# Optimization experiments

Measured on AMD Instinct MI355X. Metric: run time of the kernel, lower is better.

Reference implementation:

```python
import jax, jax.numpy as jnp
import numpy as np

B, P, K = 128, 1024, 4  # 128 clouds of 1024 points, kNN k=4 (includes self, as PyG knn does)


def _edge_mlp(e, W1, b1, W2, b2):
    # PyG MLP([2d, c, c]) with plain_last=True: ReLU after first linear only;
    # batch-norm at init (running_mean=0, var=1) is identity in eval mode.
    h = jax.nn.relu(e @ W1 + b1)
    return h @ W2 + b2


def _dynamic_edge_conv(x, W1, b1, W2, b2):
    # x: [B, P, d]. Recompute kNN graph in feature space per cloud, build edge
    # features [x_i, x_j - x_i], apply MLP, max-aggregate over neighbors.
    sq = jnp.sum(x * x, axis=-1)  # [B,P]
    dist = sq[:, :, None] + sq[:, None, :] - 2.0 * jnp.einsum('bid,bjd->bij', x, x)  # [B,P,P]
    _, idx = jax.lax.top_k(-dist, K)  # [B,P,K] nearest neighbors (self included, dist 0)
    xj = jax.vmap(lambda xc, ic: xc[ic])(x, idx)  # [B,P,K,d]
    xi = jnp.broadcast_to(x[:, :, None, :], xj.shape)
    e = jnp.concatenate([xi, xj - xi], axis=-1)  # [B,P,K,2d]
    h = _edge_mlp(e, W1, b1, W2, b2)  # [B,P,K,c]
    return jnp.max(h, axis=2)  # max aggregation -> [B,P,c]


def setup_inputs() -> dict:
    key = jax.random.key(0)
    ks = jax.random.split(key, 24)
    s = 0.1
    d = {
        'x': jax.random.normal(ks[0], (B * P, 1), dtype=jnp.float32),
        'batch': (jnp.arange(B * P, dtype=jnp.int32) // P),
        # conv1: MLP([2, 32, 32])
        'c1W1': s * jax.random.normal(ks[1], (2, 32)), 'c1b1': jnp.zeros((32,)),
        'c1W2': s * jax.random.normal(ks[2], (32, 32)), 'c1b2': jnp.zeros((32,)),
        # conv2: MLP([64, 32, 32])
        'c2W1': s * jax.random.normal(ks[3], (64, 32)), 'c2b1': jnp.zeros((32,)),
        'c2W2': s * jax.random.normal(ks[4], (32, 32)), 'c2b2': jnp.zeros((32,)),
        # conv3: MLP([64, 64, 64])
        'c3W1': s * jax.random.normal(ks[5], (64, 64)), 'c3b1': jnp.zeros((64,)),
        'c3W2': s * jax.random.normal(ks[6], (64, 64)), 'c3b2': jnp.zeros((64,)),
        # final MLP([128, 264, 264, 264, 2]), norm=None, dropout inactive in eval
        'mW1': s * jax.random.normal(ks[7], (128, 264)), 'mb1': jnp.zeros((264,)),
        'mW2': s * jax.random.normal(ks[8], (264, 264)), 'mb2': jnp.zeros((264,)),
        'mW3': s * jax.random.normal(ks[9], (264, 264)), 'mb3': jnp.zeros((264,)),
        'mW4': s * jax.random.normal(ks[10], (264, 2)), 'mb4': jnp.zeros((2,)),
    }
    return d


def reference(x, batch, c1W1, c1b1, c1W2, c1b2, c2W1, c2b1, c2W2, c2b2,
              c3W1, c3b1, c3W2, c3b2, mW1, mb1, mW2, mb2, mW3, mb3, mW4, mb4):
    # batch ids are contiguous equal-size groups (arange // P); use reshape.
    xb = x.reshape(B, P, -1)
    x1 = _dynamic_edge_conv(xb, c1W1, c1b1, c1W2, c1b2)  # [B,P,32]
    x2 = _dynamic_edge_conv(x1, c2W1, c2b1, c2W2, c2b2)  # [B,P,32]
    x3 = _dynamic_edge_conv(x2, c3W1, c3b1, c3W2, c3b2)  # [B,P,64]
    f = jnp.concatenate([x1, x2, x3], axis=-1).reshape(B * P, -1)  # [N,128]
    h = jax.nn.relu(f @ mW1 + mb1)
    h = jax.nn.relu(h @ mW2 + mb2)
    h = jax.nn.relu(h @ mW3 + mb3)
    out = h @ mW4 + mb4  # [N,2]
    return jax.nn.log_softmax(out, axis=1)
```

## Files before the change

kernel.cpp:

```cpp
#include <hip/hip_runtime.h>
#include <hip/hip_bf16.h>
#include <float.h>
#include <math.h>

#define BB 128
#define PP 1024
#define KNN 4
#define NROWS (BB * PP)

typedef __bf16 v8bf __attribute__((ext_vector_type(8)));
typedef float  v4f  __attribute__((ext_vector_type(4)));

__device__ inline unsigned short f2bs(float f) {
    __hip_bfloat16 h = __float2bfloat16(f);
    return *(unsigned short*)&h;
}
__device__ inline unsigned packbf2(float a, float b) {
    return (unsigned)f2bs(a) | ((unsigned)f2bs(b) << 16);
}
__device__ inline float bflo(unsigned u) { return __builtin_bit_cast(float, u << 16); }
__device__ inline float bfhi(unsigned u) { return __builtin_bit_cast(float, u & 0xFFFF0000u); }

__device__ inline unsigned med3u(unsigned a, unsigned b, unsigned c) {
    unsigned d;
    asm("v_med3_u32 %0, %1, %2, %3" : "=v"(d) : "v"(a), "v"(b), "v"(c));
    return d;
}

__global__ __launch_bounds__(256)
void pack_kernel(const float* __restrict__ src, int D,
                 __hip_bfloat16* __restrict__ xh, __hip_bfloat16* __restrict__ xl,
                 float* __restrict__ sq)
{
    const int t = blockIdx.x * 256 + threadIdx.x;
    const int row = t >> 2, part = t & 3;
    float v[8];
    #pragma unroll
    for (int u = 0; u < 8; u++) {
        int d = part * 8 + u;
        v[u] = (d < D) ? src[(size_t)row * D + d] : 0.f;
    }
    float s = 0.f;
    unsigned int hw[4], lw[4];
    #pragma unroll
    for (int w = 0; w < 4; w++) {
        unsigned short h2[2], l2[2];
        #pragma unroll
        for (int e = 0; e < 2; e++) {
            float x = v[2 * w + e];
            __hip_bfloat16 hb = __float2bfloat16(x);
            float hf = __bfloat162float(hb);
            __hip_bfloat16 lb = __float2bfloat16(x - hf);
            h2[e] = *(unsigned short*)&hb;
            l2[e] = *(unsigned short*)&lb;
            s = fmaf(x, x, s);
        }
        hw[w] = (unsigned int)h2[0] | ((unsigned int)h2[1] << 16);
        lw[w] = (unsigned int)l2[0] | ((unsigned int)l2[1] << 16);
    }
    s += __shfl_xor(s, 1);
    s += __shfl_xor(s, 2);
    uint4 hv; hv.x = hw[0]; hv.y = hw[1]; hv.z = hw[2]; hv.w = hw[3];
    uint4 lv; lv.x = lw[0]; lv.y = lw[1]; lv.z = lw[2]; lv.w = lw[3];
    *(uint4*)&xh[(size_t)row * 32 + part * 8] = hv;
    *(uint4*)&xl[(size_t)row * 32 + part * 8] = lv;
    if (part == 0) sq[row] = s;
}

__global__ __launch_bounds__(256, 4)
void knn_mfma(const __hip_bfloat16* __restrict__ xh, const __hip_bfloat16* __restrict__ xl,
              const float* __restrict__ sq, int* __restrict__ nidx)
{
    __shared__ __align__(16) char scb[64 * 256];
    unsigned* cand = (unsigned*)scb;

    const int tid = threadIdx.x;
    const int wv = tid >> 6, lane = tid & 63;
    const int lr = lane & 15, lq = lane >> 4;
    const int b = blockIdx.y, i0 = blockIdx.x * 64;
    const size_t Rb = (size_t)b * PP;

    v8bf ah[4], al[4];
    #pragma unroll
    for (int it = 0; it < 4; it++) {
        size_t g = Rb + i0 + it * 16 + lr;
        ah[it] = __builtin_bit_cast(v8bf, *(const uint4*)(xh + g * 32 + lq * 8));
        al[it] = __builtin_bit_cast(v8bf, *(const uint4*)(xl + g * 32 + lq * 8));
    }

    float sqq[4][4];
    #pragma unroll
    for (int it = 0; it < 4; it++)
        #pragma unroll
        for (int m = 0; m < 4; m++)
            sqq[it][m] = sq[Rb + i0 + it * 16 + lq * 4 + m];

    const int r = tid & 63, qt = tid >> 6;
    unsigned m0 = ~0u, m1 = ~0u, m2 = ~0u, m3 = ~0u;

    for (int ch = 0; ch < 8; ch++) {
        #pragma unroll
        for (int jt2 = 0; jt2 < 2; jt2++) {
            const int tl = wv * 2 + jt2;
            const size_t gj = Rb + ch * 128 + tl * 16 + lr;
            v8bf bh = __builtin_bit_cast(v8bf, *(const uint4*)(xh + gj * 32 + lq * 8));
            v8bf bl = __builtin_bit_cast(v8bf, *(const uint4*)(xl + gj * 32 + lq * 8));
            const float sqv = sq[gj];
            const unsigned jloc = (unsigned)(ch * 128 + tl * 16 + lr);
            const int cb = wv * 64 + lr * 4;
            #pragma unroll
            for (int it = 0; it < 4; it++) {
                v4f a = (v4f){0.f, 0.f, 0.f, 0.f};
                a = __builtin_amdgcn_mfma_f32_16x16x32_bf16(al[it], bl, a, 0, 0, 0);
                a = __builtin_amdgcn_mfma_f32_16x16x32_bf16(al[it], bh, a, 0, 0, 0);
                a = __builtin_amdgcn_mfma_f32_16x16x32_bf16(ah[it], bl, a, 0, 0, 0);
                a = __builtin_amdgcn_mfma_f32_16x16x32_bf16(ah[it], bh, a, 0, 0, 0);
                #pragma unroll
                for (int m = 0; m < 4; m++) {
                    float s = fmaf(-2.f, a[m], sqv + sqq[it][m]);
                    s = fmaxf(s, 0.f);
                    unsigned key = (__builtin_bit_cast(unsigned, s) & 0xFFFFFC00u) | jloc;
                    const int row = it * 16 + lq * 4 + m;
                    *(unsigned*)(scb + row * 256 + (cb ^ ((row & 7) << 4))) = key;
                }
            }
            __asm__ volatile("" ::: "memory");
            {
                const int rsw = (r & 7) << 4;
                #pragma unroll
                for (int s4 = 0; s4 < 4; s4++) {
                    uint4 kv = *(const uint4*)(scb + r * 256 + ((qt * 64 + s4 * 16) ^ rsw));
                    unsigned kk[4] = {kv.x, kv.y, kv.z, kv.w};
                    #pragma unroll
                    for (int e = 0; e < 4; e++) {
                        unsigned k = kk[e];
                        unsigned n0 = min(m0, k);
                        unsigned n1 = med3u(m0, m1, k);
                        unsigned n2 = med3u(m1, m2, k);
                        unsigned n3 = med3u(m2, m3, k);
                        m0 = n0; m1 = n1; m2 = n2; m3 = n3;
                    }
                }
            }
            __asm__ volatile("" ::: "memory");
        }
    }

    __syncthreads();
    cand[(qt * 4 + 0) * 64 + r] = m0;
    cand[(qt * 4 + 1) * 64 + r] = m1;
    cand[(qt * 4 + 2) * 64 + r] = m2;
    cand[(qt * 4 + 3) * 64 + r] = m3;
    __syncthreads();

    if (tid < 64) {
        unsigned g0 = ~0u, g1 = ~0u, g2 = ~0u, g3 = ~0u;
        #pragma unroll
        for (int s2 = 0; s2 < 16; s2++) {
            unsigned k = cand[s2 * 64 + tid];
            unsigned n0 = min(g0, k);
            unsigned n1 = med3u(g0, g1, k);
            unsigned n2 = med3u(g1, g2, k);
            unsigned n3 = med3u(g2, g3, k);
            g0 = n0; g1 = n1; g2 = n2; g3 = n3;
        }
        const int base = (int)Rb;
        int* op = nidx + (size_t)(Rb + i0 + tid) * KNN;
        op[0] = base + (int)(g0 & 1023u);
        op[1] = base + (int)(g1 & 1023u);
        op[2] = base + (int)(g2 & 1023u);
        op[3] = base + (int)(g3 & 1023u);
    }
}

template<int D, int H, int C, typename OT, bool PACK>
__global__ __launch_bounds__(256, 4)
void edge_mfma(const float* __restrict__ x, const int* __restrict__ nidx,
               const __hip_bfloat16* __restrict__ EW1, const __hip_bfloat16* __restrict__ EW2,
               const float* __restrict__ b1g, const float* __restrict__ b2g,
               OT* __restrict__ out,
               __hip_bfloat16* __restrict__ xhw, __hip_bfloat16* __restrict__ xlw,
               float* __restrict__ sqw)
{
    constexpr int NE = 256;
    constexpr int TDP = (D == 1) ? 32 : 64;
    constexpr int DP  = TDP / 2;
    constexpr int P   = ((TDP > H) ? TDP : H) + 8;
    constexpr int NT1 = H / 16, NT2 = C / 16;
    constexpr int KS1 = TDP / 32, KS2 = H / 32;

    __shared__ __hip_bfloat16 xe[NE * P];

    const int tid = threadIdx.x;
    const int wv = tid >> 6, lane = tid & 63;
    const int lr = lane & 15, q = lane >> 4;
    const int p0 = blockIdx.x * 64;

    {
        const int e = wv * 64 + lane;
        const int j = nidx[(size_t)p0 * KNN + e];
        const int pi = p0 + (e >> 2);
        if constexpr (D == 1) {
            #pragma unroll
            for (int s = 0; s < P / 8; s++) {
                uint4 z; z.x = 0u; z.y = 0u; z.z = 0u; z.w = 0u;
                *(uint4*)&xe[e * P + s * 8] = z;
            }
            xe[e * P + 0]  = __float2bfloat16(x[pi]);
            xe[e * P + DP] = __float2bfloat16(x[j]);
        } else {
            const float* si = x + (size_t)pi * D;
            const float* sj = x + (size_t)j * D;
            #pragma unroll
            for (int s = 0; s < D / 8; s++) {
                float4 f0 = *(const float4*)&si[s * 8];
                float4 f1 = *(const float4*)&si[s * 8 + 4];
                uint4 uv;
                uv.x = packbf2(f0.x, f0.y); uv.y = packbf2(f0.z, f0.w);
                uv.z = packbf2(f1.x, f1.y); uv.w = packbf2(f1.z, f1.w);
                *(uint4*)&xe[e * P + s * 8] = uv;
            }
            #pragma unroll
            for (int s = 0; s < D / 8; s++) {
                float4 f0 = *(const float4*)&sj[s * 8];
                float4 f1 = *(const float4*)&sj[s * 8 + 4];
                uint4 uv;
                uv.x = packbf2(f0.x, f0.y); uv.y = packbf2(f0.z, f0.w);
                uv.z = packbf2(f1.x, f1.y); uv.w = packbf2(f1.z, f1.w);
                *(uint4*)&xe[e * P + DP + s * 8] = uv;
            }
        }
    }

    v4f acc1[4][NT1];
    #pragma unroll
    for (int mi = 0; mi < 4; mi++)
        #pragma unroll
        for (int nt = 0; nt < NT1; nt++) acc1[mi][nt] = (v4f){0.f, 0.f, 0.f, 0.f};

    #pragma unroll
    for (int ks = 0; ks < KS1; ks++) {
        v8bf a[4];
        #pragma unroll
        for (int mi = 0; mi < 4; mi++)
            a[mi] = __builtin_bit_cast(v8bf,
                *(const uint4*)&xe[(wv * 64 + mi * 16 + lr) * P + ks * 32 + q * 8]);
        v8bf b[NT1];
        #pragma unroll
        for (int nt = 0; nt < NT1; nt++)
            b[nt] = __builtin_bit_cast(v8bf,
                *(const uint4*)(EW1 + (size_t)(nt * 16 + lr) * TDP + ks * 32 + q * 8));
        #pragma unroll
        for (int mi = 0; mi < 4; mi++)
            #pragma unroll
            for (int nt = 0; nt < NT1; nt++)
                acc1[mi][nt] = __builtin_amdgcn_mfma_f32_16x16x32_bf16(a[mi], b[nt], acc1[mi][nt], 0, 0, 0);
    }
    #pragma unroll
    for (int nt = 0; nt < NT1; nt++) {
        const float bias = b1g[nt * 16 + lr];
        #pragma unroll
        for (int mi = 0; mi < 4; mi++) {
            #pragma unroll
            for (int m = 0; m < 4; m++) {
                int row = wv * 64 + mi * 16 + q * 4 + m;
                xe[row * P + nt * 16 + lr] =
                    __float2bfloat16(fmaxf(acc1[mi][nt][m] + bias, 0.f));
            }
        }
    }

    v4f acc2[4][NT2];
    #pragma unroll
    for (int mi = 0; mi < 4; mi++)
        #pragma unroll
        for (int nt = 0; nt < NT2; nt++) acc2[mi][nt] = (v4f){0.f, 0.f, 0.f, 0.f};

    #pragma unroll
    for (int ks = 0; ks < KS2; ks++) {
        v8bf a[4];
        #pragma unroll
        for (int mi = 0; mi < 4; mi++)
            a[mi] = __builtin_bit_cast(v8bf,
                *(const uint4*)&xe[(wv * 64 + mi * 16 + lr) * P + ks * 32 + q * 8]);
        v8bf b[NT2];
        #pragma unroll
        for (int nt = 0; nt < NT2; nt++)
            b[nt] = __builtin_bit_cast(v8bf,
                *(const uint4*)(EW2 + (size_t)(nt * 16 + lr) * H + ks * 32 + q * 8));
        #pragma unroll
        for (int mi = 0; mi < 4; mi++)
            #pragma unroll
            for (int nt = 0; nt < NT2; nt++)
                acc2[mi][nt] = __builtin_amdgcn_mfma_f32_16x16x32_bf16(a[mi], b[nt], acc2[mi][nt], 0, 0, 0);
    }
    #pragma unroll
    for (int mi = 0; mi < 4; mi++) {
        const int p = p0 + (wv * 4 + mi) * 4 + q;
        float vs[NT2];
        float ss = 0.f;
        #pragma unroll
        for (int nt = 0; nt < NT2; nt++) {
            const int c = nt * 16 + lr;
            float v = fmaxf(fmaxf(acc2[mi][nt][0], acc2[mi][nt][1]),
                            fmaxf(acc2[mi][nt][2], acc2[mi][nt][3])) + b2g[c];
            vs[nt] = v;
            if constexpr (sizeof(OT) == 4) out[(size_t)p * C + c] = v;
            else                           out[(size_t)p * C + c] = __float2bfloat16(v);
            if constexpr (PACK) ss = fmaf(v, v, ss);
        }
        if constexpr (PACK) {
            ss += __shfl_xor(ss, 1);
            ss += __shfl_xor(ss, 2);
            ss += __shfl_xor(ss, 4);
            ss += __shfl_xor(ss, 8);
            #pragma unroll
            for (int nt = 0; nt < NT2; nt++) {
                float v = vs[nt];
                __hip_bfloat16 hb = __float2bfloat16(v);
                float hf = __bfloat162float(hb);
                __hip_bfloat16 lb = __float2bfloat16(v - hf);
                xhw[(size_t)p * 32 + nt * 16 + lr] = hb;
                xlw[(size_t)p * 32 + nt * 16 + lr] = lb;
            }
            if (lr == 0) sqw[p] = ss;
        }
    }
}

__global__ void prep_kernel(const float* __restrict__ mW1, const float* __restrict__ mW2,
                            const float* __restrict__ mW3,
                            const float* __restrict__ mb1, const float* __restrict__ mb2,
                            const float* __restrict__ mb3,
                            const float* __restrict__ c1W1, const float* __restrict__ c1W2,
                            const float* __restrict__ c2W1, const float* __restrict__ c2W2,
                            const float* __restrict__ c3W1, const float* __restrict__ c3W2,
                            __hip_bfloat16* __restrict__ WT1, __hip_bfloat16* __restrict__ WT2,
                            __hip_bfloat16* __restrict__ WT3, float* __restrict__ bp,
                            __hip_bfloat16* __restrict__ E11, __hip_bfloat16* __restrict__ E12,
                            __hip_bfloat16* __restrict__ E13,
                            __hip_bfloat16* __restrict__ E21, __hip_bfloat16* __restrict__ E22,
                            __hip_bfloat16* __restrict__ E23)
{
    const int t0 = blockIdx.x * blockDim.x + threadIdx.x;
    const int NT = gridDim.x * blockDim.x;
    for (int i = t0; i < 272 * 136; i += NT) {
        int n = i / 136, k = i - n * 136;
        WT1[i] = (n < 264 && k < 128) ? __float2bfloat16(mW1[(size_t)k * 264 + n]) : __float2bfloat16(0.f);
    }
    for (int i = t0; i < 272 * 296; i += NT) {
        int n = i / 296, k = i - n * 296;
        WT2[i] = (n < 264 && k < 264) ? __float2bfloat16(mW2[(size_t)k * 264 + n]) : __float2bfloat16(0.f);
        WT3[i] = (n < 264 && k < 264) ? __float2bfloat16(mW3[(size_t)k * 264 + n]) : __float2bfloat16(0.f);
    }
    for (int i = t0; i < 3 * 272; i += NT) {
        int l = i / 272, n = i - l * 272;
        const float* bsrc = (l == 0) ? mb1 : (l == 1) ? mb2 : mb3;
        bp[i] = (n < 264) ? bsrc[n] : 0.f;
    }
    for (int i = t0; i < 32 * 32; i += NT) {
        int h = i >> 5, k = i & 31;
        float v = (k == 0) ? (c1W1[h] - c1W1[32 + h]) : (k == 16 ? c1W1[32 + h] : 0.f);
        E11[i] = __float2bfloat16(v);
    }
    for (int i = t0; i < 32 * 64; i += NT) {
        int h = i >> 6, k = i & 63;
        float v = (k < 32) ? (c2W1[k * 32 + h] - c2W1[(k + 32) * 32 + h]) : c2W1[k * 32 + h];
        E12[i] = __float2bfloat16(v);
    }
    for (int i = t0; i < 64 * 64; i += NT) {
        int h = i >> 6, k = i & 63;
        float v = (k < 32) ? (c3W1[k * 64 + h] - c3W1[(k + 32) * 64 + h]) : c3W1[k * 64 + h];
        E13[i] = __float2bfloat16(v);
    }
    for (int i = t0; i < 32 * 32; i += NT) {
        int c = i >> 5, h = i & 31;
        E21[i] = __float2bfloat16(c1W2[h * 32 + c]);
        E22[i] = __float2bfloat16(c2W2[h * 32 + c]);
    }
    for (int i = t0; i < 64 * 64; i += NT) {
        int c = i >> 6, h = i & 63;
        E23[i] = __float2bfloat16(c3W2[h * 64 + c]);
    }
}

#define ACT_RB 640

template<int NK>
__device__ __forceinline__ void mlp_layer(
    char* actb, const __hip_bfloat16* __restrict__ WT, const int KP,
    const float* __restrict__ bias, const int wv, const int rlane, const int ph)
{
    v4f acc[2][4], acc16;
    #pragma unroll
    for (int i = 0; i < 2; i++)
        #pragma unroll
        for (int rt = 0; rt < 4; rt++) acc[i][rt] = (v4f){0.f, 0.f, 0.f, 0.f};
    acc16 = (v4f){0.f, 0.f, 0.f, 0.f};

    const int sw = (rlane & 7) << 4;
    const __hip_bfloat16* wbase = WT + (size_t)rlane * KP + ph * 8;
    const bool has16 = (wv >= 4);
    const int r16 = ((wv - 4) & 3) * 16 + rlane;

    v8bf wb[2][2], wb16[2];
    auto loadW = [&](int ks, int buf) {
        wb[buf][0] = __builtin_bit_cast(v8bf,
            *(const uint4*)(wbase + (size_t)wv * 16 * KP + ks * 32));
        wb[buf][1] = __builtin_bit_cast(v8bf,
            *(const uint4*)(wbase + (size_t)(8 + wv) * 16 * KP + ks * 32));
        if (has16)
            wb16[buf] = __builtin_bit_cast(v8bf,
                *(const uint4*)(wbase + (size_t)256 * KP + ks * 32));
    };
    loadW(0, 0);

    #pragma unroll
    for (int ks = 0; ks < NK; ks++) {
        const int cur = ks & 1;
        if (ks + 1 < NK) loadW(ks + 1, cur ^ 1);
        v8bf ab[4], ab16;
        #pragma unroll
        for (int rt = 0; rt < 4; rt++)
            ab[rt] = __builtin_bit_cast(v8bf,
                *(const uint4*)(actb + (rt * 16 + rlane) * ACT_RB + ((ks * 64 + ph * 16) ^ sw)));
        if (has16)
            ab16 = __builtin_bit_cast(v8bf,
                *(const uint4*)(actb + r16 * ACT_RB + ((ks * 64 + ph * 16) ^ sw)));
        #pragma unroll
        for (int i = 0; i < 2; i++)
            #pragma unroll
            for (int rt = 0; rt < 4; rt++)
                acc[i][rt] = __builtin_amdgcn_mfma_f32_16x16x32_bf16(wb[cur][i], ab[rt], acc[i][rt], 0, 0, 0);
        if (has16)
            acc16 = __builtin_amdgcn_mfma_f32_16x16x32_bf16(wb16[cur], ab16, acc16, 0, 0, 0);
    }
    __syncthreads();

    #pragma unroll
    for (int i = 0; i < 2; i++) {
        const int col0 = (wv + 8 * i) * 16 + ph * 4;
        const float4 bv = *(const float4*)&bias[col0];
        #pragma unroll
        for (int rt = 0; rt < 4; rt++) {
            const int row = rt * 16 + rlane;
            ushort4 pk;
            pk.x = f2bs(fmaxf(acc[i][rt][0] + bv.x, 0.f));
            pk.y = f2bs(fmaxf(acc[i][rt][1] + bv.y, 0.f));
            pk.z = f2bs(fmaxf(acc[i][rt][2] + bv.z, 0.f));
            pk.w = f2bs(fmaxf(acc[i][rt][3] + bv.w, 0.f));
            *(ushort4*)(actb + row * ACT_RB + ((col0 * 2) ^ ((rlane & 7) << 4))) = pk;
        }
    }
    if (has16) {
        const int col0 = 256 + ph * 4;
        const float4 bv = *(const float4*)&bias[col0];
        ushort4 pk;
        pk.x = f2bs(fmaxf(acc16[0] + bv.x, 0.f));
        pk.y = f2bs(fmaxf(acc16[1] + bv.y, 0.f));
        pk.z = f2bs(fmaxf(acc16[2] + bv.z, 0.f));
        pk.w = f2bs(fmaxf(acc16[3] + bv.w, 0.f));
        *(ushort4*)(actb + r16 * ACT_RB + ((col0 * 2) ^ ((rlane & 7) << 4))) = pk;
    }
    __syncthreads();
}

__global__ __launch_bounds__(512, 4)
void mlp_kernel(const float* __restrict__ x1, const float* __restrict__ x2,
                const __hip_bfloat16* __restrict__ x3,
                const __hip_bfloat16* __restrict__ WT1, const __hip_bfloat16* __restrict__ WT2,
                const __hip_bfloat16* __restrict__ WT3, const float* __restrict__ bp,
                const float* __restrict__ mW4, const float* __restrict__ mb4,
                float* __restrict__ outp)
{
    __shared__ __align__(16) char actb[64 * ACT_RB];
    __shared__ __align__(16) float W4s[264 * 2 + 2];
    __shared__ float lsm[512];

    const int tid = threadIdx.x;
    const int wv = tid >> 6, lane = tid & 63;
    const int rlane = lane & 15, ph = lane >> 4;
    const size_t row0 = (size_t)blockIdx.x * 64;

    {
        uint4 z; z.x = 0u; z.y = 0u; z.z = 0u; z.w = 0u;
        for (int t = tid; t < 64 * 6; t += 512) {
            int r = t / 6, s = t - r * 6;
            int cb = (34 + s) * 16;
            *(uint4*)(actb + r * ACT_RB + (cb ^ ((r & 7) << 4))) = z;
        }
        for (int t = tid; t < 64 * 8; t += 512) {
            int r = t >> 3, g = t & 7;
            size_t grow = row0 + r;
            const int swr = (r & 7) << 4;
            float4 fa = *(const float4*)&x1[grow * 32 + g * 4];
            uint2 ua; ua.x = packbf2(fa.x, fa.y); ua.y = packbf2(fa.z, fa.w);
            *(uint2*)(actb + r * ACT_RB + ((g * 8) ^ swr)) = ua;
            float4 fb = *(const float4*)&x2[grow * 32 + g * 4];
            uint2 ub; ub.x = packbf2(fb.x, fb.y); ub.y = packbf2(fb.z, fb.w);
            *(uint2*)(actb + r * ACT_RB + ((64 + g * 8) ^ swr)) = ub;
            uint4 uc = *(const uint4*)&x3[grow * 64 + g * 8];
            *(uint4*)(actb + r * ACT_RB + ((128 + g * 16) ^ swr)) = uc;
        }
        for (int t = tid; t < 530; t += 512) {
            if (t < 528) { int c = t / 264, k2 = t - c * 264; W4s[t] = mW4[(size_t)k2 * 2 + c]; }
            else W4s[t] = mb4[t - 528];
        }
    }
    __syncthreads();

    mlp_layer<4>(actb, WT1, 136, bp,       wv, rlane, ph);
    mlp_layer<9>(actb, WT2, 296, bp + 272, wv, rlane, ph);
    mlp_layer<9>(actb, WT3, 296, bp + 544, wv, rlane, ph);

    {
        const int r = tid >> 3, rem = tid & 7;
        const int c = rem >> 2, h = rem & 3;
        const float* wp = &W4s[c * 264];
        const int swr = (r & 7) << 4;
        const int k0 = (h == 0) ? 0 : (8 + 64 * h);
        const int k1 = k0 + ((h == 0) ? 72 : 64);
        float s = 0.f;
        for (int k = k0; k < k1; k += 8) {
            uint4 u = *(const uint4*)(actb + r * ACT_RB + ((2 * k) ^ swr));
            float4 wa = *(const float4*)&wp[k];
            float4 wb2 = *(const float4*)&wp[k + 4];
            s = fmaf(bflo(u.x), wa.x, s); s = fmaf(bfhi(u.x), wa.y, s);
            s = fmaf(bflo(u.y), wa.z, s); s = fmaf(bfhi(u.y), wa.w, s);
            s = fmaf(bflo(u.z), wb2.x, s); s = fmaf(bfhi(u.z), wb2.y, s);
            s = fmaf(bflo(u.w), wb2.z, s); s = fmaf(bfhi(u.w), wb2.w, s);
        }
        lsm[tid] = s;
    }
    __syncthreads();
    if (tid < 64) {
        float l0 = lsm[tid * 8 + 0] + lsm[tid * 8 + 1] + lsm[tid * 8 + 2] + lsm[tid * 8 + 3] + W4s[528];
        float l1 = lsm[tid * 8 + 4] + lsm[tid * 8 + 5] + lsm[tid * 8 + 6] + lsm[tid * 8 + 7] + W4s[529];
        float m = fmaxf(l0, l1);
        float lse = m + __logf(__expf(l0 - m) + __expf(l1 - m));
        float2 o; o.x = l0 - lse; o.y = l1 - lse;
        *(float2*)&outp[(row0 + tid) * 2] = o;
    }
}

extern "C" void kernel_launch(void* const* d_in, const int* in_sizes, int n_in,
                              void* d_out, int out_size, void* d_ws, size_t ws_size,
                              hipStream_t stream)
{
    const float* x    = (const float*)d_in[0];
    const float* c1W1 = (const float*)d_in[2];
    const float* c1b1 = (const float*)d_in[3];
    const float* c1W2 = (const float*)d_in[4];
    const float* c1b2 = (const float*)d_in[5];
    const float* c2W1 = (const float*)d_in[6];
    const float* c2b1 = (const float*)d_in[7];
    const float* c2W2 = (const float*)d_in[8];
    const float* c2b2 = (const float*)d_in[9];
    const float* c3W1 = (const float*)d_in[10];
    const float* c3b1 = (const float*)d_in[11];
    const float* c3W2 = (const float*)d_in[12];
    const float* c3b2 = (const float*)d_in[13];
    const float* mW1  = (const float*)d_in[14];
    const float* mb1  = (const float*)d_in[15];
    const float* mW2  = (const float*)d_in[16];
    const float* mb2  = (const float*)d_in[17];
    const float* mW3  = (const float*)d_in[18];
    const float* mb3  = (const float*)d_in[19];
    const float* mW4  = (const float*)d_in[20];
    const float* mb4  = (const float*)d_in[21];

    float* x1 = (float*)d_ws;
    float* x2 = x1 + (size_t)NROWS * 32;
    __hip_bfloat16* x3 = (__hip_bfloat16*)(x2 + (size_t)NROWS * 32);
    int* nidx = (int*)(x3 + (size_t)NROWS * 64);
    __hip_bfloat16* WT1 = (__hip_bfloat16*)(nidx + (size_t)NROWS * 4);
    __hip_bfloat16* WT2 = WT1 + 272 * 136;
    __hip_bfloat16* WT3 = WT2 + 272 * 296;
    float* bp = (float*)(WT3 + 272 * 296);
    __hip_bfloat16* xph = (__hip_bfloat16*)(bp + 3 * 272);
    __hip_bfloat16* xpl = xph + (size_t)NROWS * 32;
    float* sqw = (float*)(xpl + (size_t)NROWS * 32);
    __hip_bfloat16* E11 = (__hip_bfloat16*)(sqw + NROWS);
    __hip_bfloat16* E12 = E11 + 32 * 32;
    __hip_bfloat16* E13 = E12 + 32 * 64;
    __hip_bfloat16* E21 = E13 + 64 * 64;
    __hip_bfloat16* E22 = E21 + 32 * 32;
    __hip_bfloat16* E23 = E22 + 32 * 32;

    prep_kernel<<<dim3(512), 256, 0, stream>>>(mW1, mW2, mW3, mb1, mb2, mb3,
                                               c1W1, c1W2, c2W1, c2W2, c3W1, c3W2,
                                               WT1, WT2, WT3, bp,
                                               E11, E12, E13, E21, E22, E23);

    dim3 kgrid(PP / 64, BB);
    dim3 pgrid(NROWS * 4 / 256);
    dim3 egrid(NROWS / 64);

    pack_kernel<<<pgrid, 256, 0, stream>>>(x, 1, xph, xpl, sqw);
    knn_mfma<<<kgrid, 256, 0, stream>>>(xph, xpl, sqw, nidx);
    edge_mfma<1, 32, 32, float, true><<<egrid, 256, 0, stream>>>(
        x, nidx, E11, E21, c1b1, c1b2, x1, xph, xpl, sqw);

    knn_mfma<<<kgrid, 256, 0, stream>>>(xph, xpl, sqw, nidx);
    edge_mfma<32, 32, 32, float, true><<<egrid, 256, 0, stream>>>(
        x1, nidx, E12, E22, c2b1, c2b2, x2, xph, xpl, sqw);

    knn_mfma<<<kgrid, 256, 0, stream>>>(xph, xpl, sqw, nidx);
    edge_mfma<32, 64, 64, __hip_bfloat16, false><<<egrid, 256, 0, stream>>>(
        x2, nidx, E13, E23, c3b1, c3b2, x3, nullptr, nullptr, nullptr);

    mlp_kernel<<<dim3(NROWS / 64), 512, 0, stream>>>(x1, x2, x3, WT1, WT2, WT3, bp,
                                                     mW4, mb4, (float*)d_out);
}
```

Measured before the change: 394.0 us.

## Keep kNN top-4 in registers via transposed MFMA instead of LDS staging

Swaps the MFMA operand order so each lane's accumulator holds distances for a single query row across four candidates. Each lane can then keep a running top-4 per query tile in registers. The distance keys are no longer written to shared memory and re-read for insertion; per-wave candidates are merged with cross-lane shuffles and only the final lists go through LDS. This removes LDS traffic and the staging round trip, but raises register pressure (16 running minima per lane) and adds a shuffle-merge stage.

```diff
diff --git a/kernel.cpp b/kernel.cpp
--- a/kernel.cpp
+++ b/kernel.cpp
@@ -71,8 +71,7 @@
 void knn_mfma(const __hip_bfloat16* __restrict__ xh, const __hip_bfloat16* __restrict__ xl,
               const float* __restrict__ sq, int* __restrict__ nidx)
 {
-    __shared__ __align__(16) char scb[64 * 256];
-    unsigned* cand = (unsigned*)scb;
+    __shared__ unsigned cand[16 * 64];
 
     const int tid = threadIdx.x;
     const int wv = tid >> 6, lane = tid & 63;
@@ -80,77 +79,83 @@
     const int b = blockIdx.y, i0 = blockIdx.x * 64;
     const size_t Rb = (size_t)b * PP;
 
-    v8bf ah[4], al[4];
+    v8bf qh[4], ql[4];
     #pragma unroll
     for (int it = 0; it < 4; it++) {
         size_t g = Rb + i0 + it * 16 + lr;
-        ah[it] = __builtin_bit_cast(v8bf, *(const uint4*)(xh + g * 32 + lq * 8));
-        al[it] = __builtin_bit_cast(v8bf, *(const uint4*)(xl + g * 32 + lq * 8));
-    }
-
-    float sqq[4][4];
+        qh[it] = __builtin_bit_cast(v8bf, *(const uint4*)(xh + g * 32 + lq * 8));
+        ql[it] = __builtin_bit_cast(v8bf, *(const uint4*)(xl + g * 32 + lq * 8));
+    }
+    float sqq[4];
     #pragma unroll
     for (int it = 0; it < 4; it++)
-        #pragma unroll
-        for (int m = 0; m < 4; m++)
-            sqq[it][m] = sq[Rb + i0 + it * 16 + lq * 4 + m];
-
-    const int r = tid & 63, qt = tid >> 6;
-    unsigned m0 = ~0u, m1 = ~0u, m2 = ~0u, m3 = ~0u;
+        sqq[it] = sq[Rb + i0 + it * 16 + lr];
+
+    unsigned mn[4][4];
+    #pragma unroll
+    for (int it = 0; it < 4; it++)
+        #pragma unroll
+        for (int s = 0; s < 4; s++) mn[it][s] = ~0u;
 
     for (int ch = 0; ch < 8; ch++) {
         #pragma unroll
         for (int jt2 = 0; jt2 < 2; jt2++) {
-            const int tl = wv * 2 + jt2;
-            const size_t gj = Rb + ch * 128 + tl * 16 + lr;
+            const int jt = ch * 128 + (wv * 2 + jt2) * 16;
+            const size_t gj = Rb + jt + lr;
             v8bf bh = __builtin_bit_cast(v8bf, *(const uint4*)(xh + gj * 32 + lq * 8));
             v8bf bl = __builtin_bit_cast(v8bf, *(const uint4*)(xl + gj * 32 + lq * 8));
-            const float sqv = sq[gj];
-            const unsigned jloc = (unsigned)(ch * 128 + tl * 16 + lr);
-            const int cb = wv * 64 + lr * 4;
+            float4 sqc = *(const float4*)&sq[Rb + jt + lq * 4];
+            const float sqcv[4] = {sqc.x, sqc.y, sqc.z, sqc.w};
             #pragma unroll
             for (int it = 0; it < 4; it++) {
                 v4f a = (v4f){0.f, 0.f, 0.f, 0.f};
-                a = __builtin_amdgcn_mfma_f32_16x16x32_bf16(al[it], bl, a, 0, 0, 0);
-                a = __builtin_amdgcn_mfma_f32_16x16x32_bf16(al[it], bh, a, 0, 0, 0);
-                a = __builtin_amdgcn_mfma_f32_16x16x32_bf16(ah[it], bl, a, 0, 0, 0);
-                a = __builtin_amdgcn_mfma_f32_16x16x32_bf16(ah[it], bh, a, 0, 0, 0);
+                a = __builtin_amdgcn_mfma_f32_16x16x32_bf16(bl, ql[it], a, 0, 0, 0);
+                a = __builtin_amdgcn_mfma_f32_16x16x32_bf16(bl, qh[it], a, 0, 0, 0);
+                a = __builtin_amdgcn_mfma_f32_16x16x32_bf16(bh, ql[it], a, 0, 0, 0);
+                a = __builtin_amdgcn_mfma_f32_16x16x32_bf16(bh, qh[it], a, 0, 0, 0);
                 #pragma unroll
                 for (int m = 0; m < 4; m++) {
-                    float s = fmaf(-2.f, a[m], sqv + sqq[it][m]);
+                    float s = fmaf(-2.f, a[m], sqq[it] + sqcv[m]);
                     s = fmaxf(s, 0.f);
-                    unsigned key = (__builtin_bit_cast(unsigned, s) & 0xFFFFFC00u) | jloc;
-                    const int row = it * 16 + lq * 4 + m;
-                    *(unsigned*)(scb + row * 256 + (cb ^ ((row & 7) << 4))) = key;
+                    unsigned k = (__builtin_bit_cast(unsigned, s) & 0xFFFFFC00u)
+                                 | (unsigned)(jt + lq * 4 + m);
+                    unsigned n0 = min(mn[it][0], k);
+                    unsigned n1 = med3u(mn[it][0], mn[it][1], k);
+                    unsigned n2 = med3u(mn[it][1], mn[it][2], k);
+                    unsigned n3 = med3u(mn[it][2], mn[it][3], k);
+                    mn[it][0] = n0; mn[it][1] = n1; mn[it][2] = n2; mn[it][3] = n3;
                 }
             }
-            __asm__ volatile("" ::: "memory");
-            {
-                const int rsw = (r & 7) << 4;
-                #pragma unroll
-                for (int s4 = 0; s4 < 4; s4++) {
-                    uint4 kv = *(const uint4*)(scb + r * 256 + ((qt * 64 + s4 * 16) ^ rsw));
-                    unsigned kk[4] = {kv.x, kv.y, kv.z, kv.w};
-                    #pragma unroll
-                    for (int e = 0; e < 4; e++) {
-                        unsigned k = kk[e];
-                        unsigned n0 = min(m0, k);
-                        unsigned n1 = med3u(m0, m1, k);
-                        unsigned n2 = med3u(m1, m2, k);
-                        unsigned n3 = med3u(m2, m3, k);
-                        m0 = n0; m1 = n1; m2 = n2; m3 = n3;
-                    }
-                }
+        }
+    }
+
+    #pragma unroll
+    for (int d = 16; d <= 32; d <<= 1) {
+        #pragma unroll
+        for (int it = 0; it < 4; it++) {
+            unsigned o0 = __shfl_xor(mn[it][0], d);
+            unsigned o1 = __shfl_xor(mn[it][1], d);
+            unsigned o2 = __shfl_xor(mn[it][2], d);
+            unsigned o3 = __shfl_xor(mn[it][3], d);
+            #pragma unroll
+            for (int e = 0; e < 4; e++) {
+                unsigned k = (e == 0) ? o0 : (e == 1) ? o1 : (e == 2) ? o2 : o3;
+                unsigned n0 = min(mn[it][0], k);
+                unsigned n1 = med3u(mn[it][0], mn[it][1], k);
+                unsigned n2 = med3u(mn[it][1], mn[it][2], k);
+                unsigned n3 = med3u(mn[it][2], mn[it][3], k);
+                mn[it][0] = n0; mn[it][1] = n1; mn[it][2] = n2; mn[it][3] = n3;
             }
-            __asm__ volatile("" ::: "memory");
-        }
-    }
-
-    __syncthreads();
-    cand[(qt * 4 + 0) * 64 + r] = m0;
-    cand[(qt * 4 + 1) * 64 + r] = m1;
-    cand[(qt * 4 + 2) * 64 + r] = m2;
-    cand[(qt * 4 + 3) * 64 + r] = m3;
+        }
+    }
+
+    if (lane < 16) {
+        #pragma unroll
+        for (int it = 0; it < 4; it++)
+            #pragma unroll
+            for (int s = 0; s < 4; s++)
+                cand[(wv * 4 + s) * 64 + it * 16 + lr] = mn[it][s];
+    }
     __syncthreads();
 
     if (tid < 64) {
```

Result: no change. 390.1 us, median of 2 (-1.0%).
